# Optimization experiments

Hardware: AMD Instinct MI355X
Metric: run time of the kernel (lower is better)

Reference implementation:

```python
import jax, jax.numpy as jnp
import numpy as np

N_NODES = 100000
N_EDGES = 1600000
IN_DIM, HID_DIM, OUT_DIM = 32, 64, 8


def sage_conv(x, src, dst, W_l, b_l, W_r, n_nodes):
    # PyG SAGEConv (aggr='mean', root_weight=True):
    # out_i = W_l @ mean_{j in N(i)} x_j + b_l + W_r @ x_i
    msg_sum = jax.ops.segment_sum(x[src], dst, num_segments=n_nodes)  # [N, F]
    deg = jax.ops.segment_sum(jnp.ones((src.shape[0],), x.dtype), dst,
                              num_segments=n_nodes)  # [N]
    agg = msg_sum / jnp.maximum(deg, 1.0)[:, None]
    return agg @ W_l.T + b_l + x @ W_r.T


def setup_inputs() -> dict:
    key = jax.random.key(0)
    ks = jax.random.split(key, 8)
    x = jax.random.normal(ks[0], (N_NODES, IN_DIM), dtype=jnp.float32)
    edge_index = jax.random.randint(ks[1], (2, N_EDGES), 0, N_NODES, dtype=jnp.int64)
    s1 = 1.0 / np.sqrt(IN_DIM)
    s2 = 1.0 / np.sqrt(HID_DIM)
    return {
        "x": x,
        "edge_index": edge_index,
        "W1_l": jax.random.uniform(ks[2], (HID_DIM, IN_DIM), jnp.float32, -s1, s1),
        "b1": jnp.zeros((HID_DIM,), jnp.float32),
        "W1_r": jax.random.uniform(ks[3], (HID_DIM, IN_DIM), jnp.float32, -s1, s1),
        "W2_l": jax.random.uniform(ks[4], (OUT_DIM, HID_DIM), jnp.float32, -s2, s2),
        "b2": jnp.zeros((OUT_DIM,), jnp.float32),
        "W2_r": jax.random.uniform(ks[5], (OUT_DIM, HID_DIM), jnp.float32, -s2, s2),
    }


def reference(x, edge_index, W1_l, b1, W1_r, W2_l, b2, W2_r):
    src, dst = edge_index[0], edge_index[1]
    h = sage_conv(x, src, dst, W1_l, b1, W1_r, N_NODES)
    h = jax.nn.relu(h)
    out = sage_conv(h, src, dst, W2_l, b2, W2_r, N_NODES)
    return out
```

## Files before the change

### kernel.cpp

```cpp
#include <hip/hip_runtime.h>

#define N_NODES 100000
#define N_EDGES 1600000
#define IN_DIM 32
#define HID_DIM 64
#define OUT_DIM 8
#define CAP 64
#define CHUNK 4096
#define NCHUNK ((N_EDGES + CHUNK - 1) / CHUNK)
#define SLICE_W (N_NODES / 8)
#define QCAP 262144
#define BBLK 2048

typedef unsigned short u16;
typedef unsigned int u32;
typedef unsigned long long ull;

__device__ __forceinline__ float bf2f(u16 v) {
    return __uint_as_float(((u32)v) << 16);
}

__device__ __forceinline__ u16 f2bf(float f) {
    u32 u = __float_as_uint(f);
    u32 lsb = (u >> 16) & 1u;
    u += 0x7fffu + lsb;
    return (u16)(u >> 16);
}

__device__ __forceinline__ float ldf(const void* p, size_t i, int bf) {
    return bf ? bf2f(((const u16*)p)[i]) : ((const float*)p)[i];
}

__global__ __launch_bounds__(256) void k_part(
    const int* __restrict__ ei, const u32* __restrict__ xw,
    const void* __restrict__ W1l, const void* __restrict__ b1,
    const void* __restrict__ W1r,
    const void* __restrict__ W2l, const void* __restrict__ b2,
    const void* __restrict__ W2r,
    int* __restrict__ qcnt, u32* __restrict__ qbuf,
    int* __restrict__ cnt,
    float* __restrict__ tW1l, float* __restrict__ tW1r,
    float* __restrict__ tW2l, float* __restrict__ tW2r,
    float* __restrict__ tb1, float* __restrict__ tb2)
{
    __shared__ int shv, bfv;
    __shared__ int hist[4][8], wbase[4][8], lcur[4][8], gbase[8];
    int t = threadIdx.x, w = t >> 6;
    if (t < 64) {
        int v = ei[2 * t + 1];
        ull m1 = __ballot(v == 0);
        u32 wd = xw[t];
        u32 b = (wd >> 8) & 0x7fu;
        ull m2 = __ballot(b >= 0x38u && b <= 0x41u);
        if (t == 0) {
            shv = (m1 == ~0ULL) ? 1 : 0;
            bfv = (__popcll(m2) >= 56) ? 1 : 0;
        }
    }
    if (t < 32) { hist[t >> 3][t & 7] = 0; lcur[t >> 3][t & 7] = 0; }
    __syncthreads();
    int sh = shv, bf = bfv;

    for (int i = blockIdx.x * 256 + t; i < N_NODES; i += NCHUNK * 256) cnt[i] = 0;

    if (blockIdx.x < 16) {
        for (int i = blockIdx.x * 256 + t; i < HID_DIM * IN_DIM; i += 16 * 256) {
            int o = i / IN_DIM, k = i % IN_DIM;
            tW1l[k * HID_DIM + o] = ldf(W1l, i, bf);
            tW1r[k * HID_DIM + o] = ldf(W1r, i, bf);
        }
        for (int i = blockIdx.x * 256 + t; i < OUT_DIM * HID_DIM; i += 16 * 256) {
            int o = i / HID_DIM, k = i % HID_DIM;
            tW2l[k * OUT_DIM + o] = ldf(W2l, i, bf);
            tW2r[k * OUT_DIM + o] = ldf(W2r, i, bf);
        }
        if (blockIdx.x == 0) {
            if (t < HID_DIM) tb1[t] = ldf(b1, t, bf);
            if (t < OUT_DIM) tb2[t] = ldf(b2, t, bf);
        }
    }

    int e0 = blockIdx.x * CHUNK;
    int myd[16], mys[16];
    #pragma unroll
    for (int i = 0; i < 16; i++) {
        int e = e0 + i * 256 + t;
        if (e < N_EDGES) {
            size_t off = (size_t)e << sh;
            mys[i] = ei[off];
            int d = ei[((size_t)N_EDGES << sh) + off];
            myd[i] = d;
            atomicAdd(&hist[w][d / SLICE_W], 1);
        } else myd[i] = -1;
    }
    __syncthreads();
    if (t < 8) {
        int tot = hist[0][t] + hist[1][t] + hist[2][t] + hist[3][t];
        gbase[t] = atomicAdd(&qcnt[t], tot);
    }
    __syncthreads();
    if (t < 32) {
        int w2 = t >> 3, s = t & 7;
        int p = gbase[s];
        for (int w3 = 0; w3 < w2; w3++) p += hist[w3][s];
        wbase[w2][s] = p;
    }
    __syncthreads();
    #pragma unroll
    for (int i = 0; i < 16; i++) {
        int d = myd[i];
        if (d >= 0) {
            int s = d / SLICE_W;
            int p = wbase[w][s] + atomicAdd(&lcur[w][s], 1);
            qbuf[(size_t)s * QCAP + p] = ((u32)mys[i] << 14) | (u32)(d - s * SLICE_W);
        }
    }
}

__global__ __launch_bounds__(256) void k_build2(
    const int* __restrict__ qcnt, const u32* __restrict__ qbuf,
    int* __restrict__ cnt, int* __restrict__ slot)
{
    int slice = blockIdx.x & 7, bi = blockIdx.x >> 3;
    int m = qcnt[slice];
    int lo = slice * SLICE_W;
    const u32* q = qbuf + (size_t)slice * QCAP;
    for (int i = bi * 256 + threadIdx.x; i < m; i += (BBLK / 8) * 256) {
        u32 u = q[i];
        int d = lo + (int)(u & 0x3FFFu);
        int s = (int)(u >> 14);
        int pos = atomicAdd(&cnt[d], 1);
        if (pos < CAP) slot[(size_t)d * CAP + pos] = s;
    }
}

__global__ __launch_bounds__(256, 8) void k_sage1(
    const void* __restrict__ x, const int* __restrict__ cnt,
    const int* __restrict__ slot,
    const float* __restrict__ tW1l, const float* __restrict__ tW1r,
    const float* __restrict__ tW2l, const float* __restrict__ tW2r,
    const float* __restrict__ tb1, const float* __restrict__ tb2,
    const int* __restrict__ flags_unused,
    u16* __restrict__ gbuf, float* __restrict__ rbuf,
    const u32* __restrict__ xw)
{
    __shared__ float aggbuf[8][IN_DIM];
    __shared__ float xbuf[8][IN_DIM];
    __shared__ float hbuf[8][HID_DIM + 1];
    __shared__ int bfv;

    int t = threadIdx.x;
    if (t < 64) {
        u32 wd = xw[t];
        u32 b = (wd >> 8) & 0x7fu;
        ull m2 = __ballot(b >= 0x38u && b <= 0x41u);
        if (t == 0) bfv = (__popcll(m2) >= 56) ? 1 : 0;
    }
    __syncthreads();
    int bf = bfv;
    int wid = t >> 6, lane = t & 63;
    int half = lane >> 5;
    int g2 = (lane >> 3) & 3;
    int l = lane & 7;
    int ns = wid * 2 + half;
    int n = blockIdx.x * 8 + ns;
    int deg = cnt[n];
    int cl = (deg < CAP) ? deg : CAP;
    const int* srow = slot + (size_t)n * CAP;

    float a0 = 0, a1 = 0, a2 = 0, a3 = 0;
    float c0 = 0, c1 = 0, c2 = 0, c3 = 0;
    float d0 = 0, d1 = 0, d2 = 0, d3 = 0;
    float e0 = 0, e1 = 0, e2 = 0, e3 = 0;
    int j = g2;
    for (; j + 12 < cl; j += 16) {
        int sA = srow[j];
        int sB = srow[j + 4];
        int sC = srow[j + 8];
        int sD = srow[j + 12];
        if (bf) {
            ushort4 vA = reinterpret_cast<const ushort4*>((const u16*)x + (size_t)sA * IN_DIM)[l];
            ushort4 vB = reinterpret_cast<const ushort4*>((const u16*)x + (size_t)sB * IN_DIM)[l];
            ushort4 vC = reinterpret_cast<const ushort4*>((const u16*)x + (size_t)sC * IN_DIM)[l];
            ushort4 vD = reinterpret_cast<const ushort4*>((const u16*)x + (size_t)sD * IN_DIM)[l];
            a0 += bf2f(vA.x); a1 += bf2f(vA.y); a2 += bf2f(vA.z); a3 += bf2f(vA.w);
            c0 += bf2f(vB.x); c1 += bf2f(vB.y); c2 += bf2f(vB.z); c3 += bf2f(vB.w);
            d0 += bf2f(vC.x); d1 += bf2f(vC.y); d2 += bf2f(vC.z); d3 += bf2f(vC.w);
            e0 += bf2f(vD.x); e1 += bf2f(vD.y); e2 += bf2f(vD.z); e3 += bf2f(vD.w);
        } else {
            float4 vA = reinterpret_cast<const float4*>((const float*)x + (size_t)sA * IN_DIM)[l];
            float4 vB = reinterpret_cast<const float4*>((const float*)x + (size_t)sB * IN_DIM)[l];
            float4 vC = reinterpret_cast<const float4*>((const float*)x + (size_t)sC * IN_DIM)[l];
            float4 vD = reinterpret_cast<const float4*>((const float*)x + (size_t)sD * IN_DIM)[l];
            a0 += vA.x; a1 += vA.y; a2 += vA.z; a3 += vA.w;
            c0 += vB.x; c1 += vB.y; c2 += vB.z; c3 += vB.w;
            d0 += vC.x; d1 += vC.y; d2 += vC.z; d3 += vC.w;
            e0 += vD.x; e1 += vD.y; e2 += vD.z; e3 += vD.w;
        }
    }
    for (; j + 4 < cl; j += 8) {
        int sA = srow[j];
        int sB = srow[j + 4];
        if (bf) {
            ushort4 vA = reinterpret_cast<const ushort4*>((const u16*)x + (size_t)sA * IN_DIM)[l];
            ushort4 vB = reinterpret_cast<const ushort4*>((const u16*)x + (size_t)sB * IN_DIM)[l];
            a0 += bf2f(vA.x); a1 += bf2f(vA.y); a2 += bf2f(vA.z); a3 += bf2f(vA.w);
            c0 += bf2f(vB.x); c1 += bf2f(vB.y); c2 += bf2f(vB.z); c3 += bf2f(vB.w);
        } else {
            float4 vA = reinterpret_cast<const float4*>((const float*)x + (size_t)sA * IN_DIM)[l];
            float4 vB = reinterpret_cast<const float4*>((const float*)x + (size_t)sB * IN_DIM)[l];
            a0 += vA.x; a1 += vA.y; a2 += vA.z; a3 += vA.w;
            c0 += vB.x; c1 += vB.y; c2 += vB.z; c3 += vB.w;
        }
    }
    if (j < cl) {
        int s = srow[j];
        if (bf) {
            ushort4 v = reinterpret_cast<const ushort4*>((const u16*)x + (size_t)s * IN_DIM)[l];
            a0 += bf2f(v.x); a1 += bf2f(v.y); a2 += bf2f(v.z); a3 += bf2f(v.w);
        } else {
            float4 v = reinterpret_cast<const float4*>((const float*)x + (size_t)s * IN_DIM)[l];
            a0 += v.x; a1 += v.y; a2 += v.z; a3 += v.w;
        }
    }
    a0 += c0 + d0 + e0;
    a1 += c1 + d1 + e1;
    a2 += c2 + d2 + e2;
    a3 += c3 + d3 + e3;
    a0 += __shfl_xor(a0, 8, 64);  a0 += __shfl_xor(a0, 16, 64);
    a1 += __shfl_xor(a1, 8, 64);  a1 += __shfl_xor(a1, 16, 64);
    a2 += __shfl_xor(a2, 8, 64);  a2 += __shfl_xor(a2, 16, 64);
    a3 += __shfl_xor(a3, 8, 64);  a3 += __shfl_xor(a3, 16, 64);
    if (g2 == 0) {
        aggbuf[ns][4 * l + 0] = a0; aggbuf[ns][4 * l + 1] = a1;
        aggbuf[ns][4 * l + 2] = a2; aggbuf[ns][4 * l + 3] = a3;
    } else if (g2 == 1) {
        float f0, f1, f2, f3;
        if (bf) {
            ushort4 v = reinterpret_cast<const ushort4*>((const u16*)x + (size_t)n * IN_DIM)[l];
            f0 = bf2f(v.x); f1 = bf2f(v.y); f2 = bf2f(v.z); f3 = bf2f(v.w);
        } else {
            float4 v = reinterpret_cast<const float4*>((const float*)x + (size_t)n * IN_DIM)[l];
            f0 = v.x; f1 = v.y; f2 = v.z; f3 = v.w;
        }
        xbuf[ns][4 * l + 0] = f0; xbuf[ns][4 * l + 1] = f1;
        xbuf[ns][4 * l + 2] = f2; xbuf[ns][4 * l + 3] = f3;
    }
    __syncthreads();

    float rd0 = 1.0f / fmaxf((float)__shfl(deg, 0, 64), 1.0f);
    float rd1 = 1.0f / fmaxf((float)__shfl(deg, 32, 64), 1.0f);
    int s0 = wid * 2, s1 = wid * 2 + 1;
    int o = lane;
    float bb = tb1[o];
    float acc0 = bb, acc1 = bb;
    #pragma unroll 8
    for (int k = 0; k < IN_DIM; k++) {
        float wl = tW1l[k * HID_DIM + o];
        float wr = tW1r[k * HID_DIM + o];
        acc0 += (aggbuf[s0][k] * rd0) * wl + xbuf[s0][k] * wr;
        acc1 += (aggbuf[s1][k] * rd1) * wl + xbuf[s1][k] * wr;
    }
    hbuf[s0][o] = fmaxf(acc0, 0.0f);
    hbuf[s1][o] = fmaxf(acc1, 0.0f);
    __syncthreads();

    float ga = 0.0f, ra = 0.0f;
    #pragma unroll 4
    for (int m = 0; m < 16; m++) {
        int k = g2 * 16 + m;
        float hv = hbuf[ns][k];
        ga += hv * tW2l[k * OUT_DIM + l];
        ra += hv * tW2r[k * OUT_DIM + l];
    }
    ga += __shfl_xor(ga, 8, 64);  ga += __shfl_xor(ga, 16, 64);
    ra += __shfl_xor(ra, 8, 64);  ra += __shfl_xor(ra, 16, 64);
    if (g2 == 0) {
        gbuf[(size_t)n * OUT_DIM + l] = f2bf(ga);
        rbuf[(size_t)n * OUT_DIM + l] = ra + tb2[l];
    }
}

__global__ __launch_bounds__(256) void k_sage3(
    const u16* __restrict__ gbuf, const float* __restrict__ rbuf,
    const int* __restrict__ cnt, const int* __restrict__ slot,
    const u32* __restrict__ xw, void* __restrict__ out)
{
    __shared__ int bfv;
    int t = threadIdx.x;
    if (t < 64) {
        u32 w = xw[t];
        u32 b = (w >> 8) & 0x7fu;
        ull m2 = __ballot(b >= 0x38u && b <= 0x41u);
        if (t == 0) bfv = (__popcll(m2) >= 56) ? 1 : 0;
    }
    __syncthreads();
    int grp = t >> 3, l = t & 7;
    int n = blockIdx.x * 32 + grp;
    int deg = cnt[n];
    int cl = (deg < CAP) ? deg : CAP;
    const int* srow = slot + (size_t)n * CAP;
    float a0 = 0.0f, a1 = 0.0f, a2 = 0.0f, a3 = 0.0f;
    int j = 0;
    for (; j + 3 < cl; j += 4) {
        int v0 = srow[j];
        int v1 = srow[j + 1];
        int v2 = srow[j + 2];
        int v3 = srow[j + 3];
        a0 += bf2f(gbuf[(size_t)v0 * OUT_DIM + l]);
        a1 += bf2f(gbuf[(size_t)v1 * OUT_DIM + l]);
        a2 += bf2f(gbuf[(size_t)v2 * OUT_DIM + l]);
        a3 += bf2f(gbuf[(size_t)v3 * OUT_DIM + l]);
    }
    for (; j < cl; j++) a0 += bf2f(gbuf[(size_t)srow[j] * OUT_DIM + l]);
    float res = (a0 + a1 + a2 + a3) / fmaxf((float)deg, 1.0f)
              + rbuf[(size_t)n * OUT_DIM + l];
    size_t oi = (size_t)n * OUT_DIM + l;
    if (bfv) ((u16*)out)[oi] = f2bf(res);
    else     ((float*)out)[oi] = res;
}

extern "C" void kernel_launch(void* const* d_in, const int* in_sizes, int n_in,
                              void* d_out, int out_size, void* d_ws, size_t ws_size,
                              hipStream_t stream) {
    const void* x   = d_in[0];
    const int*  ei  = (const int*)d_in[1];
    const void* W1l = d_in[2];
    const void* b1  = d_in[3];
    const void* W1r = d_in[4];
    const void* W2l = d_in[5];
    const void* b2  = d_in[6];
    const void* W2r = d_in[7];

    int* qcnt    = (int*)d_ws;
    int* cnt     = qcnt + 8;
    float* tW1l  = (float*)(cnt + N_NODES);
    float* tW1r  = tW1l + IN_DIM * HID_DIM;
    float* tW2l  = tW1r + IN_DIM * HID_DIM;
    float* tW2r  = tW2l + HID_DIM * OUT_DIM;
    float* tb1   = tW2r + HID_DIM * OUT_DIM;
    float* tb2   = tb1 + HID_DIM;
    int* slot    = (int*)(tb2 + OUT_DIM);
    u32* qbuf    = (u32*)(slot + (size_t)N_NODES * CAP);
    u16* gbuf    = (u16*)(qbuf + (size_t)8 * QCAP);
    float* rbuf  = (float*)(gbuf + (size_t)N_NODES * OUT_DIM);

    hipMemsetAsync(d_ws, 0, 8 * sizeof(int), stream);

    k_part<<<NCHUNK, 256, 0, stream>>>(ei, (const u32*)x,
                                       W1l, b1, W1r, W2l, b2, W2r,
                                       qcnt, qbuf, cnt,
                                       tW1l, tW1r, tW2l, tW2r, tb1, tb2);
    k_build2<<<BBLK, 256, 0, stream>>>(qcnt, qbuf, cnt, slot);
    k_sage1<<<N_NODES / 8, 256, 0, stream>>>(x, cnt, slot, tW1l, tW1r,
                                             tW2l, tW2r, tb1, tb2, nullptr,
                                             gbuf, rbuf, (const u32*)x);
    k_sage3<<<N_NODES / 32, 256, 0, stream>>>(gbuf, rbuf, cnt, slot,
                                              (const u32*)x, d_out);
}
```

Before: 254.0 us.

## Split layer-1 aggregation into two feature-half passes over column-split copies of x

Splits x into low and high 16-feature halves stored as separate contiguous arrays, then runs the neighbor-mean gather twice, once per half. Each pass touches a gather working set half the size, meant to fit better in cache and cut random-access misses. A separate dense kernel then reads the aggregated means and does both matmuls. The cost is an extra copy of x, reading the slot lists twice, an extra kernel launch, and the aggregates making a round trip through global memory.

```diff
diff --git a/kernel.cpp b/kernel.cpp
--- a/kernel.cpp
+++ b/kernel.cpp
@@ -15,6 +15,7 @@
 typedef unsigned short u16;
 typedef unsigned int u32;
 typedef unsigned long long ull;
+typedef float f4 __attribute__((ext_vector_type(4)));
 
 __device__ __forceinline__ float bf2f(u16 v) {
     return __uint_as_float(((u32)v) << 16);
@@ -41,7 +42,8 @@
     int* __restrict__ cnt,
     float* __restrict__ tW1l, float* __restrict__ tW1r,
     float* __restrict__ tW2l, float* __restrict__ tW2r,
-    float* __restrict__ tb1, float* __restrict__ tb2)
+    float* __restrict__ tb1, float* __restrict__ tb2,
+    u32* __restrict__ xlo, u32* __restrict__ xhi)
 {
     __shared__ int shv, bfv;
     __shared__ int hist[4][8], wbase[4][8], lcur[4][8], gbase[8];
@@ -62,6 +64,20 @@
     int sh = shv, bf = bfv;
 
     for (int i = blockIdx.x * 256 + t; i < N_NODES; i += NCHUNK * 256) cnt[i] = 0;
+
+    if (bf) {
+        for (int i = blockIdx.x * 256 + t; i < N_NODES * 8; i += NCHUNK * 256) {
+            int n2 = i >> 3, k = i & 7;
+            xlo[i] = xw[n2 * 16 + k];
+            xhi[i] = xw[n2 * 16 + 8 + k];
+        }
+    } else {
+        for (int i = blockIdx.x * 256 + t; i < N_NODES * 16; i += NCHUNK * 256) {
+            int n2 = i >> 4, k = i & 15;
+            xlo[i] = xw[n2 * 32 + k];
+            xhi[i] = xw[n2 * 32 + 16 + k];
+        }
+    }
 
     if (blockIdx.x < 16) {
         for (int i = blockIdx.x * 256 + t; i < HID_DIM * IN_DIM; i += 16 * 256) {
@@ -134,21 +150,12 @@
     }
 }
 
-__global__ __launch_bounds__(256, 8) void k_sage1(
-    const void* __restrict__ x, const int* __restrict__ cnt,
-    const int* __restrict__ slot,
-    const float* __restrict__ tW1l, const float* __restrict__ tW1r,
-    const float* __restrict__ tW2l, const float* __restrict__ tW2r,
-    const float* __restrict__ tb1, const float* __restrict__ tb2,
-    const int* __restrict__ flags_unused,
-    u16* __restrict__ gbuf, float* __restrict__ rbuf,
+__global__ __launch_bounds__(256) void k_agg(
+    const void* __restrict__ xh, const int* __restrict__ cnt,
+    const int* __restrict__ slot, float* __restrict__ agg,
     const u32* __restrict__ xw)
 {
-    __shared__ float aggbuf[8][IN_DIM];
-    __shared__ float xbuf[8][IN_DIM];
-    __shared__ float hbuf[8][HID_DIM + 1];
     __shared__ int bfv;
-
     int t = threadIdx.x;
     if (t < 64) {
         u32 wd = xw[t];
@@ -160,8 +167,8 @@
     int bf = bfv;
     int wid = t >> 6, lane = t & 63;
     int half = lane >> 5;
-    int g2 = (lane >> 3) & 3;
-    int l = lane & 7;
+    int m = lane & 31;
+    int g = m >> 2, l = m & 3;
     int ns = wid * 2 + half;
     int n = blockIdx.x * 8 + ns;
     int deg = cnt[n];
@@ -170,86 +177,92 @@
 
     float a0 = 0, a1 = 0, a2 = 0, a3 = 0;
     float c0 = 0, c1 = 0, c2 = 0, c3 = 0;
-    float d0 = 0, d1 = 0, d2 = 0, d3 = 0;
-    float e0 = 0, e1 = 0, e2 = 0, e3 = 0;
-    int j = g2;
-    for (; j + 12 < cl; j += 16) {
-        int sA = srow[j];
-        int sB = srow[j + 4];
-        int sC = srow[j + 8];
-        int sD = srow[j + 12];
+    int j = g;
+    for (; j + 8 < cl; j += 16) {
+        int sA = __builtin_nontemporal_load(&srow[j]);
+        int sB = __builtin_nontemporal_load(&srow[j + 8]);
         if (bf) {
-            ushort4 vA = reinterpret_cast<const ushort4*>((const u16*)x + (size_t)sA * IN_DIM)[l];
-            ushort4 vB = reinterpret_cast<const ushort4*>((const u16*)x + (size_t)sB * IN_DIM)[l];
-            ushort4 vC = reinterpret_cast<const ushort4*>((const u16*)x + (size_t)sC * IN_DIM)[l];
-            ushort4 vD = reinterpret_cast<const ushort4*>((const u16*)x + (size_t)sD * IN_DIM)[l];
-            a0 += bf2f(vA.x); a1 += bf2f(vA.y); a2 += bf2f(vA.z); a3 += bf2f(vA.w);
-            c0 += bf2f(vB.x); c1 += bf2f(vB.y); c2 += bf2f(vB.z); c3 += bf2f(vB.w);
-            d0 += bf2f(vC.x); d1 += bf2f(vC.y); d2 += bf2f(vC.z); d3 += bf2f(vC.w);
-            e0 += bf2f(vD.x); e1 += bf2f(vD.y); e2 += bf2f(vD.z); e3 += bf2f(vD.w);
-        } else {
-            float4 vA = reinterpret_cast<const float4*>((const float*)x + (size_t)sA * IN_DIM)[l];
-            float4 vB = reinterpret_cast<const float4*>((const float*)x + (size_t)sB * IN_DIM)[l];
-            float4 vC = reinterpret_cast<const float4*>((const float*)x + (size_t)sC * IN_DIM)[l];
-            float4 vD = reinterpret_cast<const float4*>((const float*)x + (size_t)sD * IN_DIM)[l];
-            a0 += vA.x; a1 += vA.y; a2 += vA.z; a3 += vA.w;
-            c0 += vB.x; c1 += vB.y; c2 += vB.z; c3 += vB.w;
-            d0 += vC.x; d1 += vC.y; d2 += vC.z; d3 += vC.w;
-            e0 += vD.x; e1 += vD.y; e2 += vD.z; e3 += vD.w;
-        }
-    }
-    for (; j + 4 < cl; j += 8) {
-        int sA = srow[j];
-        int sB = srow[j + 4];
-        if (bf) {
-            ushort4 vA = reinterpret_cast<const ushort4*>((const u16*)x + (size_t)sA * IN_DIM)[l];
-            ushort4 vB = reinterpret_cast<const ushort4*>((const u16*)x + (size_t)sB * IN_DIM)[l];
+            ushort4 vA = reinterpret_cast<const ushort4*>((const u16*)xh + (size_t)sA * 16)[l];
+            ushort4 vB = reinterpret_cast<const ushort4*>((const u16*)xh + (size_t)sB * 16)[l];
             a0 += bf2f(vA.x); a1 += bf2f(vA.y); a2 += bf2f(vA.z); a3 += bf2f(vA.w);
             c0 += bf2f(vB.x); c1 += bf2f(vB.y); c2 += bf2f(vB.z); c3 += bf2f(vB.w);
         } else {
-            float4 vA = reinterpret_cast<const float4*>((const float*)x + (size_t)sA * IN_DIM)[l];
-            float4 vB = reinterpret_cast<const float4*>((const float*)x + (size_t)sB * IN_DIM)[l];
+            float4 vA = reinterpret_cast<const float4*>((const float*)xh + (size_t)sA * 16)[l];
+            float4 vB = reinterpret_cast<const float4*>((const float*)xh + (size_t)sB * 16)[l];
             a0 += vA.x; a1 += vA.y; a2 += vA.z; a3 += vA.w;
             c0 += vB.x; c1 += vB.y; c2 += vB.z; c3 += vB.w;
         }
     }
     if (j < cl) {
-        int s = srow[j];
+        int s = __builtin_nontemporal_load(&srow[j]);
         if (bf) {
-            ushort4 v = reinterpret_cast<const ushort4*>((const u16*)x + (size_t)s * IN_DIM)[l];
+            ushort4 v = reinterpret_cast<const ushort4*>((const u16*)xh + (size_t)s * 16)[l];
             a0 += bf2f(v.x); a1 += bf2f(v.y); a2 += bf2f(v.z); a3 += bf2f(v.w);
         } else {
-            float4 v = reinterpret_cast<const float4*>((const float*)x + (size_t)s * IN_DIM)[l];
+            float4 v = reinterpret_cast<const float4*>((const float*)xh + (size_t)s * 16)[l];
             a0 += v.x; a1 += v.y; a2 += v.z; a3 += v.w;
         }
     }
-    a0 += c0 + d0 + e0;
-    a1 += c1 + d1 + e1;
-    a2 += c2 + d2 + e2;
-    a3 += c3 + d3 + e3;
-    a0 += __shfl_xor(a0, 8, 64);  a0 += __shfl_xor(a0, 16, 64);
-    a1 += __shfl_xor(a1, 8, 64);  a1 += __shfl_xor(a1, 16, 64);
-    a2 += __shfl_xor(a2, 8, 64);  a2 += __shfl_xor(a2, 16, 64);
-    a3 += __shfl_xor(a3, 8, 64);  a3 += __shfl_xor(a3, 16, 64);
-    if (g2 == 0) {
-        aggbuf[ns][4 * l + 0] = a0; aggbuf[ns][4 * l + 1] = a1;
-        aggbuf[ns][4 * l + 2] = a2; aggbuf[ns][4 * l + 3] = a3;
-    } else if (g2 == 1) {
-        float f0, f1, f2, f3;
+    a0 += c0; a1 += c1; a2 += c2; a3 += c3;
+    a0 += __shfl_xor(a0, 4, 64); a0 += __shfl_xor(a0, 8, 64); a0 += __shfl_xor(a0, 16, 64);
+    a1 += __shfl_xor(a1, 4, 64); a1 += __shfl_xor(a1, 8, 64); a1 += __shfl_xor(a1, 16, 64);
+    a2 += __shfl_xor(a2, 4, 64); a2 += __shfl_xor(a2, 8, 64); a2 += __shfl_xor(a2, 16, 64);
+    a3 += __shfl_xor(a3, 4, 64); a3 += __shfl_xor(a3, 8, 64); a3 += __shfl_xor(a3, 16, 64);
+    if (g == 0) {
+        float rd = 1.0f / fmaxf((float)deg, 1.0f);
+        f4 o;
+        o.x = a0 * rd; o.y = a1 * rd; o.z = a2 * rd; o.w = a3 * rd;
+        __builtin_nontemporal_store(o, reinterpret_cast<f4*>(agg + (size_t)n * 16) + l);
+    }
+}
+
+__global__ __launch_bounds__(256, 8) void k_dense(
+    const void* __restrict__ x,
+    const float* __restrict__ agglo, const float* __restrict__ agghi,
+    const float* __restrict__ tW1l, const float* __restrict__ tW1r,
+    const float* __restrict__ tW2l, const float* __restrict__ tW2r,
+    const float* __restrict__ tb1, const float* __restrict__ tb2,
+    u16* __restrict__ gbuf, float* __restrict__ rbuf,
+    const u32* __restrict__ xw)
+{
+    __shared__ float aggbuf[8][IN_DIM];
+    __shared__ float xbuf[8][IN_DIM];
+    __shared__ float hbuf[8][HID_DIM + 1];
+    __shared__ int bfv;
+
+    int t = threadIdx.x;
+    if (t < 64) {
+        u32 wd = xw[t];
+        u32 b = (wd >> 8) & 0x7fu;
+        ull m2 = __ballot(b >= 0x38u && b <= 0x41u);
+        if (t == 0) bfv = (__popcll(m2) >= 56) ? 1 : 0;
+    }
+    __syncthreads();
+    int bf = bfv;
+    int nb = blockIdx.x * 8;
+
+    {
+        int ks = t >> 5, k = t & 31;
+        int n = nb + ks;
+        aggbuf[ks][k] = (k < 16) ? agglo[(size_t)n * 16 + k]
+                                 : agghi[(size_t)n * 16 + (k - 16)];
+    }
+    if (t < 64) {
+        int ks = t >> 3, l = t & 7;
+        int n = nb + ks;
         if (bf) {
             ushort4 v = reinterpret_cast<const ushort4*>((const u16*)x + (size_t)n * IN_DIM)[l];
-            f0 = bf2f(v.x); f1 = bf2f(v.y); f2 = bf2f(v.z); f3 = bf2f(v.w);
+            xbuf[ks][4 * l + 0] = bf2f(v.x); xbuf[ks][4 * l + 1] = bf2f(v.y);
+            xbuf[ks][4 * l + 2] = bf2f(v.z); xbuf[ks][4 * l + 3] = bf2f(v.w);
         } else {
             float4 v = reinterpret_cast<const float4*>((const float*)x + (size_t)n * IN_DIM)[l];
-            f0 = v.x; f1 = v.y; f2 = v.z; f3 = v.w;
-        }
-        xbuf[ns][4 * l + 0] = f0; xbuf[ns][4 * l + 1] = f1;
-        xbuf[ns][4 * l + 2] = f2; xbuf[ns][4 * l + 3] = f3;
-    }
-    __syncthreads();
-
-    float rd0 = 1.0f / fmaxf((float)__shfl(deg, 0, 64), 1.0f);
-    float rd1 = 1.0f / fmaxf((float)__shfl(deg, 32, 64), 1.0f);
+            xbuf[ks][4 * l + 0] = v.x; xbuf[ks][4 * l + 1] = v.y;
+            xbuf[ks][4 * l + 2] = v.z; xbuf[ks][4 * l + 3] = v.w;
+        }
+    }
+    __syncthreads();
+
+    int wid = t >> 6, lane = t & 63;
     int s0 = wid * 2, s1 = wid * 2 + 1;
     int o = lane;
     float bb = tb1[o];
@@ -258,17 +271,20 @@
     for (int k = 0; k < IN_DIM; k++) {
         float wl = tW1l[k * HID_DIM + o];
         float wr = tW1r[k * HID_DIM + o];
-        acc0 += (aggbuf[s0][k] * rd0) * wl + xbuf[s0][k] * wr;
-        acc1 += (aggbuf[s1][k] * rd1) * wl + xbuf[s1][k] * wr;
+        acc0 += aggbuf[s0][k] * wl + xbuf[s0][k] * wr;
+        acc1 += aggbuf[s1][k] * wl + xbuf[s1][k] * wr;
     }
     hbuf[s0][o] = fmaxf(acc0, 0.0f);
     hbuf[s1][o] = fmaxf(acc1, 0.0f);
     __syncthreads();
 
+    int half = lane >> 5, g2 = (lane >> 3) & 3, l = lane & 7;
+    int ns = wid * 2 + half;
+    int n = nb + ns;
     float ga = 0.0f, ra = 0.0f;
     #pragma unroll 4
-    for (int m = 0; m < 16; m++) {
-        int k = g2 * 16 + m;
+    for (int mm = 0; mm < 16; mm++) {
+        int k = g2 * 16 + mm;
         float hv = hbuf[ns][k];
         ga += hv * tW2l[k * OUT_DIM + l];
         ra += hv * tW2r[k * OUT_DIM + l];
@@ -342,18 +358,25 @@
     float* tb2   = tb1 + HID_DIM;
     int* slot    = (int*)(tb2 + OUT_DIM);
     u32* qbuf    = (u32*)(slot + (size_t)N_NODES * CAP);
-    u16* gbuf    = (u16*)(qbuf + (size_t)8 * QCAP);
+    float* agglo = (float*)qbuf;
+    float* agghi = agglo + (size_t)N_NODES * 16;
+    u16* gbuf    = (u16*)(agghi + (size_t)N_NODES * 16);
     float* rbuf  = (float*)(gbuf + (size_t)N_NODES * OUT_DIM);
+    u32* xlo     = (u32*)(rbuf + (size_t)N_NODES * OUT_DIM);
+    u32* xhi     = xlo + (size_t)N_NODES * 16;
 
     hipMemsetAsync(d_ws, 0, 8 * sizeof(int), stream);
 
     k_part<<<NCHUNK, 256, 0, stream>>>(ei, (const u32*)x,
                                        W1l, b1, W1r, W2l, b2, W2r,
                                        qcnt, qbuf, cnt,
-                                       tW1l, tW1r, tW2l, tW2r, tb1, tb2);
+                                       tW1l, tW1r, tW2l, tW2r, tb1, tb2,
+                                       xlo, xhi);
     k_build2<<<BBLK, 256, 0, stream>>>(qcnt, qbuf, cnt, slot);
-    k_sage1<<<N_NODES / 8, 256, 0, stream>>>(x, cnt, slot, tW1l, tW1r,
-                                             tW2l, tW2r, tb1, tb2, nullptr,
+    k_agg<<<N_NODES / 8, 256, 0, stream>>>(xlo, cnt, slot, agglo, (const u32*)x);
+    k_agg<<<N_NODES / 8, 256, 0, stream>>>(xhi, cnt, slot, agghi, (const u32*)x);
+    k_dense<<<N_NODES / 8, 256, 0, stream>>>(x, agglo, agghi,
+                                             tW1l, tW1r, tW2l, tW2r, tb1, tb2,
                                              gbuf, rbuf, (const u32*)x);
     k_sage3<<<N_NODES / 32, 256, 0, stream>>>(gbuf, rbuf, cnt, slot,
                                               (const u32*)x, d_out);
```

Measured after the change: 294.8 us. +16.0%, slower.

## Replace fixed-capacity neighbor slots with exact CSR built via degree prefix scan

Applied to the files above, without the earlier changes.

Degrees are now counted during partitioning, and a two-level prefix scan produces per-node offsets. Neighbor sources are scattered into a compact CSR array instead of a padded 64-slot-per-node table. This shrinks the neighbor-list footprint and makes the gather reads contiguous, and it also removes the degree cap, which was a correctness risk for nodes above 64 neighbors. In exchange it adds two scan launches, a larger memset, an extra atomic per edge in the partition kernel, and extra offset loads in every consumer kernel.

```diff
diff --git a/kernel.cpp b/kernel.cpp
--- a/kernel.cpp
+++ b/kernel.cpp
@@ -1,16 +1,17 @@
 #include <hip/hip_runtime.h>
 
 #define N_NODES 100000
+#define N_PAD 100352
 #define N_EDGES 1600000
 #define IN_DIM 32
 #define HID_DIM 64
 #define OUT_DIM 8
-#define CAP 64
 #define CHUNK 4096
 #define NCHUNK ((N_EDGES + CHUNK - 1) / CHUNK)
 #define SLICE_W (N_NODES / 8)
 #define QCAP 262144
 #define BBLK 2048
+#define SCAN_B (N_PAD / 256)
 
 typedef unsigned short u16;
 typedef unsigned int u32;
@@ -61,8 +62,6 @@
     __syncthreads();
     int sh = shv, bf = bfv;
 
-    for (int i = blockIdx.x * 256 + t; i < N_NODES; i += NCHUNK * 256) cnt[i] = 0;
-
     if (blockIdx.x < 16) {
         for (int i = blockIdx.x * 256 + t; i < HID_DIM * IN_DIM; i += 16 * 256) {
             int o = i / IN_DIM, k = i % IN_DIM;
@@ -91,6 +90,7 @@
             int d = ei[((size_t)N_EDGES << sh) + off];
             myd[i] = d;
             atomicAdd(&hist[w][d / SLICE_W], 1);
+            atomicAdd(&cnt[d], 1);
         } else myd[i] = -1;
     }
     __syncthreads();
@@ -117,30 +117,75 @@
     }
 }
 
+__global__ __launch_bounds__(256) void k_scan1(
+    const int* __restrict__ cnt, int* __restrict__ off, int* __restrict__ bsum)
+{
+    int t = threadIdx.x, b = blockIdx.x;
+    int i = b * 256 + t;
+    int v = cnt[i];
+    int lane = t & 63, w = t >> 6;
+    int inc = v;
+    #pragma unroll
+    for (int o = 1; o < 64; o <<= 1) {
+        int y = __shfl_up(inc, o, 64);
+        if (lane >= o) inc += y;
+    }
+    __shared__ int wsum[4];
+    if (lane == 63) wsum[w] = inc;
+    __syncthreads();
+    int base = 0;
+    #pragma unroll
+    for (int k = 0; k < 4; k++) if (k < w) base += wsum[k];
+    off[i] = base + inc - v;
+    if (t == 255) bsum[b] = base + inc;
+}
+
+__global__ __launch_bounds__(512) void k_scan2(
+    const int* __restrict__ bsum, int* __restrict__ boff)
+{
+    int t = threadIdx.x;
+    int v = (t < SCAN_B) ? bsum[t] : 0;
+    int lane = t & 63, w = t >> 6;
+    int inc = v;
+    #pragma unroll
+    for (int o = 1; o < 64; o <<= 1) {
+        int y = __shfl_up(inc, o, 64);
+        if (lane >= o) inc += y;
+    }
+    __shared__ int wsum[8];
+    if (lane == 63) wsum[w] = inc;
+    __syncthreads();
+    int base = 0;
+    #pragma unroll
+    for (int k = 0; k < 8; k++) if (k < w) base += wsum[k];
+    if (t < SCAN_B) boff[t] = base + inc - v;
+}
+
 __global__ __launch_bounds__(256) void k_build2(
     const int* __restrict__ qcnt, const u32* __restrict__ qbuf,
-    int* __restrict__ cnt, int* __restrict__ slot)
+    const int* __restrict__ off, const int* __restrict__ boff,
+    int* __restrict__ cnt2, int* __restrict__ csr)
 {
     int slice = blockIdx.x & 7, bi = blockIdx.x >> 3;
     int m = qcnt[slice];
     int lo = slice * SLICE_W;
     const u32* q = qbuf + (size_t)slice * QCAP;
     for (int i = bi * 256 + threadIdx.x; i < m; i += (BBLK / 8) * 256) {
-        u32 u = q[i];
+        u32 u = __builtin_nontemporal_load(&q[i]);
         int d = lo + (int)(u & 0x3FFFu);
         int s = (int)(u >> 14);
-        int pos = atomicAdd(&cnt[d], 1);
-        if (pos < CAP) slot[(size_t)d * CAP + pos] = s;
+        int pos = off[d] + boff[d >> 8] + atomicAdd(&cnt2[d], 1);
+        csr[pos] = s;
     }
 }
 
 __global__ __launch_bounds__(256, 8) void k_sage1(
     const void* __restrict__ x, const int* __restrict__ cnt,
-    const int* __restrict__ slot,
+    const int* __restrict__ csr,
+    const int* __restrict__ off, const int* __restrict__ boff,
     const float* __restrict__ tW1l, const float* __restrict__ tW1r,
     const float* __restrict__ tW2l, const float* __restrict__ tW2r,
     const float* __restrict__ tb1, const float* __restrict__ tb2,
-    const int* __restrict__ flags_unused,
     u16* __restrict__ gbuf, float* __restrict__ rbuf,
     const u32* __restrict__ xw)
 {
@@ -165,8 +210,8 @@
     int ns = wid * 2 + half;
     int n = blockIdx.x * 8 + ns;
     int deg = cnt[n];
-    int cl = (deg < CAP) ? deg : CAP;
-    const int* srow = slot + (size_t)n * CAP;
+    int cl = deg;
+    const int* srow = csr + off[n] + boff[n >> 8];
 
     float a0 = 0, a1 = 0, a2 = 0, a3 = 0;
     float c0 = 0, c1 = 0, c2 = 0, c3 = 0;
@@ -283,7 +328,8 @@
 
 __global__ __launch_bounds__(256) void k_sage3(
     const u16* __restrict__ gbuf, const float* __restrict__ rbuf,
-    const int* __restrict__ cnt, const int* __restrict__ slot,
+    const int* __restrict__ cnt, const int* __restrict__ csr,
+    const int* __restrict__ off, const int* __restrict__ boff,
     const u32* __restrict__ xw, void* __restrict__ out)
 {
     __shared__ int bfv;
@@ -298,8 +344,8 @@
     int grp = t >> 3, l = t & 7;
     int n = blockIdx.x * 32 + grp;
     int deg = cnt[n];
-    int cl = (deg < CAP) ? deg : CAP;
-    const int* srow = slot + (size_t)n * CAP;
+    int cl = deg;
+    const int* srow = csr + off[n] + boff[n >> 8];
     float a0 = 0.0f, a1 = 0.0f, a2 = 0.0f, a3 = 0.0f;
     int j = 0;
     for (; j + 3 < cl; j += 4) {
@@ -334,27 +380,33 @@
 
     int* qcnt    = (int*)d_ws;
     int* cnt     = qcnt + 8;
-    float* tW1l  = (float*)(cnt + N_NODES);
+    int* cnt2    = cnt + N_PAD;
+    int* off     = cnt2 + N_PAD;
+    int* bsum    = off + N_PAD;
+    int* boff    = bsum + 512;
+    float* tW1l  = (float*)(boff + 512);
     float* tW1r  = tW1l + IN_DIM * HID_DIM;
     float* tW2l  = tW1r + IN_DIM * HID_DIM;
     float* tW2r  = tW2l + HID_DIM * OUT_DIM;
     float* tb1   = tW2r + HID_DIM * OUT_DIM;
     float* tb2   = tb1 + HID_DIM;
-    int* slot    = (int*)(tb2 + OUT_DIM);
-    u32* qbuf    = (u32*)(slot + (size_t)N_NODES * CAP);
+    int* csr     = (int*)(tb2 + OUT_DIM);
+    u32* qbuf    = (u32*)(csr + N_EDGES);
     u16* gbuf    = (u16*)(qbuf + (size_t)8 * QCAP);
     float* rbuf  = (float*)(gbuf + (size_t)N_NODES * OUT_DIM);
 
-    hipMemsetAsync(d_ws, 0, 8 * sizeof(int), stream);
+    hipMemsetAsync(d_ws, 0, (8 + 2 * N_PAD) * sizeof(int), stream);
 
     k_part<<<NCHUNK, 256, 0, stream>>>(ei, (const u32*)x,
                                        W1l, b1, W1r, W2l, b2, W2r,
                                        qcnt, qbuf, cnt,
                                        tW1l, tW1r, tW2l, tW2r, tb1, tb2);
-    k_build2<<<BBLK, 256, 0, stream>>>(qcnt, qbuf, cnt, slot);
-    k_sage1<<<N_NODES / 8, 256, 0, stream>>>(x, cnt, slot, tW1l, tW1r,
-                                             tW2l, tW2r, tb1, tb2, nullptr,
+    k_scan1<<<SCAN_B, 256, 0, stream>>>(cnt, off, bsum);
+    k_scan2<<<1, 512, 0, stream>>>(bsum, boff);
+    k_build2<<<BBLK, 256, 0, stream>>>(qcnt, qbuf, off, boff, cnt2, csr);
+    k_sage1<<<N_NODES / 8, 256, 0, stream>>>(x, cnt, csr, off, boff,
+                                             tW1l, tW1r, tW2l, tW2r, tb1, tb2,
                                              gbuf, rbuf, (const u32*)x);
-    k_sage3<<<N_NODES / 32, 256, 0, stream>>>(gbuf, rbuf, cnt, slot,
+    k_sage3<<<N_NODES / 32, 256, 0, stream>>>(gbuf, rbuf, cnt, csr, off, boff,
                                               (const u32*)x, d_out);
 }
```

Measured after the change: 315.0 us. 1.24x slower.
